# Kernel optimization log

Measured on AMD Instinct MI355X. Metric: run time of the kernel, lower is better.

The kernel has to match this reference:

```python
import jax, jax.numpy as jnp
import numpy as np

R = 15  # receptive-field rows (self.rfield)
_NAMES = ['1x', '2x', '3x', '4x', '1e', '2e', '3e', '4e', '5', '6', '7', '8', '9']
_CIN = [3, 64, 64, 64, 3, 64, 64, 64, 64, 64, 64, 64, 64]
_COUT = [64, 64, 64, 64, 64, 64, 64, 64, 64, 64, 64, 64, 3]


def _leaky(x):
    return jnp.where(x >= 0, x, 0.01 * x)  # nn.LeakyReLU default slope


def _conv(x, w, b, ph):
    # 3x3 conv, stride 1, padding (ph, 1) matching torch Conv2d padding=[ph, 1]
    y = jax.lax.conv_general_dilated(x, w, (1, 1), ((ph, ph), (1, 1)),
                                     dimension_numbers=('NCHW', 'OIHW', 'NCHW'))
    return y + b[None, :, None, None]


def setup_inputs():
    key = jax.random.key(0)
    ks = jax.random.split(key, len(_NAMES) + 1)
    inp = {'x': jax.random.normal(ks[0], (1, 3, 31, 256), jnp.float32)}
    for j, n in enumerate(_NAMES):
        std = np.float32((2.0 / (_CIN[j] * 9)) ** 0.5)  # He init for 3x3 conv
        inp['w' + n] = jax.random.normal(ks[j + 1], (_COUT[j], _CIN[j], 3, 3), jnp.float32) * std
        inp['b' + n] = jnp.zeros((_COUT[j],), jnp.float32)
    return inp


def _predict(s, e, p):
    # x-branch: 15 rows -> 9 rows (three H-valid convs)
    for n, ph in (('1x', 1), ('2x', 0), ('3x', 0), ('4x', 0)):
        s = _leaky(_conv(s, p['w' + n], p['b' + n], ph))
    # e-branch
    for n, ph in (('1e', 1), ('2e', 0), ('3e', 0), ('4e', 0)):
        e = _leaky(_conv(e, p['w' + n], p['b' + n], ph))
    B, C, Hs, W = s.shape  # C == 64 -> per-pixel 8x8 matrices; Hs == R - 6 == 9
    sr = jnp.transpose(s, (0, 2, 3, 1)).reshape(B, Hs, W, 8, 8)
    er = jnp.transpose(e, (0, 2, 3, 1)).reshape(B, Hs, W, 8, 8)
    pr = jnp.einsum('bhwij,bhwjk->bhwik', er, sr).reshape(B, Hs, W, 64)
    pr = jnp.transpose(pr, (0, 3, 1, 2))  # [B,64,9,W]
    # fuse stack: 9 rows -> 1 row, then 64 -> 3 channels
    for n, ph in (('5', 0), ('6', 0), ('7', 0), ('8', 0), ('9', 1)):
        pr = _leaky(_conv(pr, p['w' + n], p['b' + n], ph))
    return pr  # [B, 3, 1, W]


def _forward(x, p):
    B, C, H, W = x.shape

    def step(ebuf, i):
        # torch code sets error = x (alias), so slice_x and slice_e are the SAME mutated buffer
        sl = jax.lax.dynamic_slice(ebuf, (0, 0, i, 0), (B, C, R, W))
        pr = _predict(sl, sl, p)
        # act_row reads row ky of the (mutated) x, but row ky is overwritten only after this read,
        # so it still equals the original input row
        act = jax.lax.dynamic_slice(x, (0, 0, i + R, 0), (B, C, 1, W))
        ebuf = jax.lax.dynamic_update_slice(ebuf, act - pr, (0, 0, i + R, 0))
        return ebuf, pr

    ebuf, preds = jax.lax.scan(step, x, jnp.arange(H - R))
    pred = jnp.transpose(preds[:, :, :, 0, :], (1, 2, 0, 3))  # [S,B,C,1,W] -> [B,C,S,W]
    # 'truth' is read from the in-place-mutated x, i.e. the residual buffer, matching the torch aliasing bug/behavior
    truth = ebuf[:, :, R:, :]
    return pred, truth


def reference(x, w1x, b1x, w2x, b2x, w3x, b3x, w4x, b4x, w1e, b1e, w2e, b2e, w3e, b3e, w4e, b4e, w5, b5, w6, b6, w7, b7, w8, b8, w9, b9):
    p = dict(w1x=w1x, b1x=b1x, w2x=w2x, b2x=b2x, w3x=w3x, b3x=b3x, w4x=w4x, b4x=b4x,
             w1e=w1e, b1e=b1e, w2e=w2e, b2e=b2e, w3e=w3e, b3e=b3e, w4e=w4e, b4e=b4e,
             w5=w5, b5=b5, w6=w6, b6=b6, w7=w7, b7=b7, w8=w8, b8=b8, w9=w9, b9=b9)
    return _forward(x, p)
```

## Files before the change

kernel.cpp:

```cpp
#include <hip/hip_runtime.h>

#define LEAKY(v) ((v) >= 0.f ? (v) : 0.01f * (v))

#define CS   4608
#define ZS1  294912
#define TSL  16
#define BSL  17
#define EBCS 7936

struct JobD { const float* t0; const float* t1; const float* t2; float* o; };
struct IncP { JobD jd[6]; };

__global__ __launch_bounds__(256, 2) void convInc(
    IncP P, const float* __restrict__ W0, const float* __restrict__ B0,
    const float* __restrict__ W1, const float* __restrict__ B1,
    int zsel, int ics, int ocs)
{
    const int lane = threadIdx.x;
    const int y    = threadIdx.y;
    const int q    = blockIdx.x >> 6;
    const int cout = blockIdx.x & 63;
    const int z    = (zsel >> q) & 1;
    const float* W  = (z ? W1 : W0) + cout * 576 + y * 144;
    const float* Bv = z ? B1 : B0;
    const JobD jd  = P.jd[q];
    const int yo   = y * 16 * ics + lane * 4;
    const float* t0 = jd.t0 + yo;
    const float* t1 = jd.t1 + yo;
    const float* t2 = jd.t2 + yo;

    float acc[4] = {};
    #pragma unroll 4
    for (int c = 0; c < 16; ++c) {
        #pragma unroll
        for (int t = 0; t < 3; ++t) {
            const float* rp = (t == 0 ? t0 : (t == 1 ? t1 : t2)) + c * ics;
            float4 v = *(const float4*)rp;
            float wl = __shfl_up(v.w, 1);   if (lane == 0)  wl = 0.f;
            float wr = __shfl_down(v.x, 1); if (lane == 63) wr = 0.f;
            const float win[6] = {wl, v.x, v.y, v.z, v.w, wr};
            const float* wj = W + c * 9 + t * 3;
            #pragma unroll
            for (int cc = 0; cc < 4; ++cc)
                acc[cc] += wj[0] * win[cc] + wj[1] * win[cc + 1] + wj[2] * win[cc + 2];
        }
    }

    __shared__ float red[4][256];
    *(float4*)&red[y][lane * 4] = *(float4*)acc;
    __syncthreads();
    const int col = y * 64 + lane;
    float v = Bv[cout] + red[0][col] + red[1][col] + red[2][col] + red[3][col];
    jd.o[cout * ocs + col] = LEAKY(v);
}

struct C3P { const float* t[3][3]; float* o[3][2]; };

__global__ __launch_bounds__(256, 2) void conv3inc(
    C3P P, const float* __restrict__ W0, const float* __restrict__ B0,
    const float* __restrict__ W1, const float* __restrict__ B1)
{
    const int lane = threadIdx.x & 63;
    const int wv   = threadIdx.x >> 6;
    const int job  = blockIdx.x >> 3;
    const int cq   = blockIdx.x & 3;
    const int z    = (blockIdx.x >> 2) & 1;
    const int cout0 = __builtin_amdgcn_readfirstlane(cq * 16 + wv * 4);
    const float* W  = (z ? W1 : W0) + cout0 * 27;
    const float* Bv = z ? B1 : B0;

    float a[4][4] = {};
    #pragma unroll
    for (int t = 0; t < 3; ++t) {
        const float* rp = P.t[job][t];
        if (rp) {
            #pragma unroll
            for (int c = 0; c < 3; ++c) {
                float4 v = *(const float4*)(rp + c * EBCS + lane * 4);
                float wl = __shfl_up(v.w, 1);   if (lane == 0)  wl = 0.f;
                float wr = __shfl_down(v.x, 1); if (lane == 63) wr = 0.f;
                const float win[6] = {wl, v.x, v.y, v.z, v.w, wr};
                #pragma unroll
                for (int j = 0; j < 4; ++j) {
                    const float* wj = W + j * 27 + c * 9 + t * 3;
                    #pragma unroll
                    for (int cc = 0; cc < 4; ++cc)
                        a[j][cc] += wj[0] * win[cc] + wj[1] * win[cc + 1] + wj[2] * win[cc + 2];
                }
            }
        }
    }
    float* o = P.o[job][z];
    #pragma unroll
    for (int j = 0; j < 4; ++j) {
        const float bb = Bv[cout0 + j];
        float4 r4;
        r4.x = LEAKY(a[j][0] + bb); r4.y = LEAKY(a[j][1] + bb);
        r4.z = LEAKY(a[j][2] + bb); r4.w = LEAKY(a[j][3] + bb);
        *(float4*)(o + (cout0 + j) * CS + lane * 4) = r4;
    }
}

__global__ __launch_bounds__(256, 2) void conv3B(
    const float* __restrict__ ebuf,
    const float* __restrict__ W0, const float* __restrict__ B0,
    const float* __restrict__ W1, const float* __restrict__ B1,
    float* __restrict__ out)
{
    const int lane = threadIdx.x & 63;
    const int wv   = threadIdx.x >> 6;
    const int h  = blockIdx.y;
    const int cq = blockIdx.z & 3;
    const int z  = blockIdx.z >> 2;
    const int cout0 = __builtin_amdgcn_readfirstlane(cq * 16 + wv * 4);
    const float* W  = (z ? W1 : W0) + cout0 * 27;
    const float* Bv = z ? B1 : B0;

    float a[4][4] = {};
    #pragma unroll
    for (int kh = 0; kh < 3; ++kh) {
        const int r = h - 1 + kh;
        const bool valid = (r >= 0 && r < 15);
        const float msk = valid ? 1.f : 0.f;
        #pragma unroll
        for (int c = 0; c < 3; ++c) {
            const float* rr = ebuf + c * EBCS + (valid ? r : 0) * 256 + lane * 4;
            float4 v = *(const float4*)rr;
            v.x *= msk; v.y *= msk; v.z *= msk; v.w *= msk;
            float wl = __shfl_up(v.w, 1);   if (lane == 0)  wl = 0.f;
            float wr = __shfl_down(v.x, 1); if (lane == 63) wr = 0.f;
            const float win[6] = {wl, v.x, v.y, v.z, v.w, wr};
            #pragma unroll
            for (int j = 0; j < 4; ++j) {
                const float* wj = W + j * 27 + c * 9 + kh * 3;
                #pragma unroll
                for (int cc = 0; cc < 4; ++cc)
                    a[j][cc] += wj[0] * win[cc] + wj[1] * win[cc + 1] + wj[2] * win[cc + 2];
            }
        }
    }
    const int slot = (h == 0) ? TSL : (h == 14 ? BSL : (h & 15));
    float* o = out + (size_t)z * ZS1 + slot * 256;
    #pragma unroll
    for (int j = 0; j < 4; ++j) {
        const float bb = Bv[cout0 + j];
        float4 r4;
        r4.x = LEAKY(a[j][0] + bb); r4.y = LEAKY(a[j][1] + bb);
        r4.z = LEAKY(a[j][2] + bb); r4.w = LEAKY(a[j][3] + bb);
        *(float4*)(o + (cout0 + j) * CS + lane * 4) = r4;
    }
}

template<int HOUT, int HIN, int OFFI, int OFFO, int NZ>
__global__ __launch_bounds__(256, 2) void convYB(
    const float* __restrict__ in,
    const float* __restrict__ W0, const float* __restrict__ B0,
    const float* __restrict__ W1, const float* __restrict__ B1,
    float* __restrict__ out)
{
    const int lane = threadIdx.x;
    const int y    = threadIdx.y;
    const int h  = blockIdx.y;
    const int gz = blockIdx.z;
    const int z    = (NZ == 2) ? (gz >> 6) : 0;
    const int cout = (NZ == 2) ? (gz & 63) : gz;
    const float* W  = (z ? W1 : W0) + cout * 576 + y * 144;
    const float* Bv = z ? B1 : B0;
    const float* ib = in + (size_t)z * ZS1 + y * 16 * CS + lane * 4;

    int slot[3];
    #pragma unroll
    for (int t = 0; t < 3; ++t) {
        const int g = h + t;
        slot[t] = (g == 0) ? TSL : (g == HIN - 1 ? BSL : ((g + OFFI) & 15));
    }

    float acc[4] = {};
    #pragma unroll 4
    for (int c = 0; c < 16; ++c) {
        #pragma unroll
        for (int t = 0; t < 3; ++t) {
            float4 v = *(const float4*)(ib + c * CS + slot[t] * 256);
            float wl = __shfl_up(v.w, 1);   if (lane == 0)  wl = 0.f;
            float wr = __shfl_down(v.x, 1); if (lane == 63) wr = 0.f;
            const float win[6] = {wl, v.x, v.y, v.z, v.w, wr};
            const float* wj = W + c * 9 + t * 3;
            #pragma unroll
            for (int cc = 0; cc < 4; ++cc)
                acc[cc] += wj[0] * win[cc] + wj[1] * win[cc + 1] + wj[2] * win[cc + 2];
        }
    }

    __shared__ float red[4][256];
    *(float4*)&red[y][lane * 4] = *(float4*)acc;
    __syncthreads();
    const int col = y * 64 + lane;
    const int os = (h == 0) ? TSL : (h == HOUT - 1 ? BSL : ((h + OFFO) & 15));
    float v = Bv[cout] + red[0][col] + red[1][col] + red[2][col] + red[3][col];
    out[(size_t)z * ZS1 + cout * CS + os * 256 + col] = LEAKY(v);
}

__global__ __launch_bounds__(256, 2) void mmB(const float* __restrict__ L4R,
                                              float* __restrict__ MMR)
{
    const int col = threadIdx.x;
    const int r   = blockIdx.x;
    const int ig  = blockIdx.y;
    const int slot = (r == 0) ? TSL : (r == 8 ? BSL : ((r + 3) & 15));
    const float* s = L4R + slot * 256 + col;
    const float* e = L4R + ZS1 + slot * 256 + col;
    float sv[64];
    #pragma unroll
    for (int c = 0; c < 64; ++c) sv[c] = s[c * CS];
    float ev[8];
    #pragma unroll
    for (int j = 0; j < 8; ++j) ev[j] = e[(ig * 8 + j) * CS];
    #pragma unroll
    for (int k = 0; k < 8; ++k) {
        float acc = 0.f;
        #pragma unroll
        for (int j = 0; j < 8; ++j) acc += ev[j] * sv[j * 8 + k];
        MMR[(ig * 8 + k) * CS + slot * 256 + col] = acc;
    }
}

struct MMP { const float* s[3]; const float* e[3]; float* o[3]; };
__global__ __launch_bounds__(256, 2) void mminc(MMP P)
{
    const int col = threadIdx.x;
    const int job = blockIdx.x;
    const int ig  = blockIdx.y;
    const float* s = P.s[job] + col;
    const float* e = P.e[job] + col;
    float sv[64];
    #pragma unroll
    for (int c = 0; c < 64; ++c) sv[c] = s[c * CS];
    float ev[8];
    #pragma unroll
    for (int j = 0; j < 8; ++j) ev[j] = e[(ig * 8 + j) * CS];
    float* o = P.o[job];
    #pragma unroll
    for (int k = 0; k < 8; ++k) {
        float acc = 0.f;
        #pragma unroll
        for (int j = 0; j < 8; ++j) acc += ev[j] * sv[j * 8 + k];
        o[(ig * 8 + k) * CS + col] = acc;
    }
}

__global__ void conv9up(const float* __restrict__ pin, const float* __restrict__ w9,
                        const float* __restrict__ b9, const float* __restrict__ x,
                        float* __restrict__ ebuf, float* __restrict__ preds, int i)
{
    const int wcol = threadIdx.x;
    const int yq   = threadIdx.y;
    const int c0   = yq * 16;
    const bool mL = (wcol > 0), mR = (wcol < 255);
    float a0 = 0.f, a1 = 0.f, a2 = 0.f;

    #pragma unroll 4
    for (int c = 0; c < 16; ++c) {
        const int cin = c0 + c;
        const float* r_ = pin + cin * 256;
        float vm = mL ? r_[wcol - 1] : 0.f;
        float v0 = r_[wcol];
        float vp = mR ? r_[wcol + 1] : 0.f;
        const float* wk0 = w9 + (0 * 64 + cin) * 9 + 3;
        const float* wk1 = w9 + (1 * 64 + cin) * 9 + 3;
        const float* wk2 = w9 + (2 * 64 + cin) * 9 + 3;
        a0 += vm * wk0[0] + v0 * wk0[1] + vp * wk0[2];
        a1 += vm * wk1[0] + v0 * wk1[1] + vp * wk1[2];
        a2 += vm * wk2[0] + v0 * wk2[1] + vp * wk2[2];
    }

    __shared__ float red[4][3][256];
    red[yq][0][wcol] = a0;
    red[yq][1][wcol] = a1;
    red[yq][2][wcol] = a2;
    __syncthreads();

    if (yq == 0) {
        #pragma unroll
        for (int j = 0; j < 3; ++j) {
            float v = b9[j] + red[0][j][wcol] + red[1][j][wcol]
                            + red[2][j][wcol] + red[3][j][wcol];
            v = LEAKY(v);
            preds[i * 768 + j * 256 + wcol] = v;
            ebuf[j * EBCS + (15 + i) * 256 + wcol] =
                x[j * EBCS + (15 + i) * 256 + wcol] - v;
        }
    }
}

__global__ void finalize(const float* __restrict__ preds, const float* __restrict__ ebuf,
                         float* __restrict__ o)
{
    const int idx = blockIdx.x * 256 + threadIdx.x;
    if (idx >= 24576) return;
    if (idx < 12288) {
        const int c = idx >> 12;
        const int t = (idx >> 8) & 15;
        const int w = idx & 255;
        o[idx] = preds[t * 768 + c * 256 + w];
    } else {
        const int j = idx - 12288;
        const int c = j >> 12;
        const int t = (j >> 8) & 15;
        const int w = j & 255;
        o[idx] = ebuf[c * EBCS + (15 + t) * 256 + w];
    }
}

extern "C" void kernel_launch(void* const* d_in, const int* in_sizes, int n_in,
                              void* d_out, int out_size, void* d_ws, size_t ws_size,
                              hipStream_t stream)
{
    const float* x   = (const float*)d_in[0];
    const float* w1x = (const float*)d_in[1];  const float* b1x = (const float*)d_in[2];
    const float* w2x = (const float*)d_in[3];  const float* b2x = (const float*)d_in[4];
    const float* w3x = (const float*)d_in[5];  const float* b3x = (const float*)d_in[6];
    const float* w4x = (const float*)d_in[7];  const float* b4x = (const float*)d_in[8];
    const float* w1e = (const float*)d_in[9];  const float* b1e = (const float*)d_in[10];
    const float* w2e = (const float*)d_in[11]; const float* b2e = (const float*)d_in[12];
    const float* w3e = (const float*)d_in[13]; const float* b3e = (const float*)d_in[14];
    const float* w4e = (const float*)d_in[15]; const float* b4e = (const float*)d_in[16];
    const float* w5  = (const float*)d_in[17]; const float* b5  = (const float*)d_in[18];
    const float* w6  = (const float*)d_in[19]; const float* b6  = (const float*)d_in[20];
    const float* w7  = (const float*)d_in[21]; const float* b7  = (const float*)d_in[22];
    const float* w8  = (const float*)d_in[23]; const float* b8  = (const float*)d_in[24];
    const float* w9  = (const float*)d_in[25]; const float* b9  = (const float*)d_in[26];

    float* ws    = (float*)d_ws;
    float* ebuf  = ws;
    float* L1R   = ebuf + 23808;
    float* L2R   = L1R + 589824;
    float* L3R   = L2R + 589824;
    float* L4R   = L3R + 589824;
    float* MMR   = L4R + 589824;
    float* L5R   = MMR + 294912;
    float* L6R   = L5R + 294912;
    float* L7b   = L6R + 294912;
    float* L8b   = L7b + 49152;
    float* preds = L8b + 16384;

    auto S2 = [](int c) { return c & 15; };
    auto r2 = [](float* b, int z, int slot) { return b + (size_t)z * ZS1 + slot * 256; };
    auto r1 = [](float* b, int slot) { return b + slot * 256; };

    hipMemcpyAsync(ebuf, x, 23808 * sizeof(float), hipMemcpyDeviceToDevice, stream);

    const dim3 cb(64, 4);

    conv3B<<<dim3(1, 15, 8), 256, 0, stream>>>(ebuf, w1x, b1x, w1e, b1e, L1R);
    convYB<13, 15, 0, 1, 2><<<dim3(1, 13, 128), cb, 0, stream>>>(L1R, w2x, b2x, w2e, b2e, L2R);
    convYB<11, 13, 1, 2, 2><<<dim3(1, 11, 128), cb, 0, stream>>>(L2R, w3x, b3x, w3e, b3e, L3R);
    convYB<9, 11, 2, 3, 2><<<dim3(1, 9, 128), cb, 0, stream>>>(L3R, w4x, b4x, w4e, b4e, L4R);
    mmB<<<dim3(9, 8), 256, 0, stream>>>(L4R, MMR);
    convYB<7, 9, 3, 4, 1><<<dim3(1, 7, 64), cb, 0, stream>>>(MMR, w5, b5, w5, b5, L5R);
    convYB<5, 7, 4, 5, 1><<<dim3(1, 5, 64), cb, 0, stream>>>(L5R, w6, b6, w6, b6, L6R);

    for (int i = 0; i < 16; ++i) {
        if (i > 0) {
            C3P p3 = {};
            p3.t[0][0] = nullptr;                p3.t[0][1] = ebuf + i * 256;        p3.t[0][2] = ebuf + (i + 1) * 256;
            p3.t[1][0] = ebuf + (i + 13) * 256;  p3.t[1][1] = ebuf + (i + 14) * 256; p3.t[1][2] = nullptr;
            p3.t[2][0] = ebuf + (i + 12) * 256;  p3.t[2][1] = ebuf + (i + 13) * 256; p3.t[2][2] = ebuf + (i + 14) * 256;
            for (int z = 0; z < 2; ++z) {
                p3.o[0][z] = r2(L1R, z, TSL);
                p3.o[1][z] = r2(L1R, z, BSL);
                p3.o[2][z] = r2(L1R, z, S2(i + 13));
            }
            conv3inc<<<24, 256, 0, stream>>>(p3, w1x, b1x, w1e, b1e);

            IncP p2 = {};
            for (int z = 0; z < 2; ++z) {
                p2.jd[0 * 2 + z] = { r2(L1R, z, TSL),        r2(L1R, z, S2(i + 1)),  r2(L1R, z, S2(i + 2)),  r2(L2R, z, TSL) };
                p2.jd[1 * 2 + z] = { r2(L1R, z, S2(i + 12)), r2(L1R, z, S2(i + 13)), r2(L1R, z, BSL),        r2(L2R, z, BSL) };
                p2.jd[2 * 2 + z] = { r2(L1R, z, S2(i + 11)), r2(L1R, z, S2(i + 12)), r2(L1R, z, S2(i + 13)), r2(L2R, z, S2(i + 12)) };
            }
            convInc<<<384, cb, 0, stream>>>(p2, w2x, b2x, w2e, b2e, 42, CS, CS);

            IncP p3i = {};
            for (int z = 0; z < 2; ++z) {
                p3i.jd[0 * 2 + z] = { r2(L2R, z, TSL),        r2(L2R, z, S2(i + 2)),  r2(L2R, z, S2(i + 3)),  r2(L3R, z, TSL) };
                p3i.jd[1 * 2 + z] = { r2(L2R, z, S2(i + 11)), r2(L2R, z, S2(i + 12)), r2(L2R, z, BSL),        r2(L3R, z, BSL) };
                p3i.jd[2 * 2 + z] = { r2(L2R, z, S2(i + 10)), r2(L2R, z, S2(i + 11)), r2(L2R, z, S2(i + 12)), r2(L3R, z, S2(i + 11)) };
            }
            convInc<<<384, cb, 0, stream>>>(p3i, w3x, b3x, w3e, b3e, 42, CS, CS);

            IncP p4 = {};
            for (int z = 0; z < 2; ++z) {
                p4.jd[0 * 2 + z] = { r2(L3R, z, TSL),        r2(L3R, z, S2(i + 3)),  r2(L3R, z, S2(i + 4)),  r2(L4R, z, TSL) };
                p4.jd[1 * 2 + z] = { r2(L3R, z, S2(i + 10)), r2(L3R, z, S2(i + 11)), r2(L3R, z, BSL),        r2(L4R, z, BSL) };
                p4.jd[2 * 2 + z] = { r2(L3R, z, S2(i + 9)),  r2(L3R, z, S2(i + 10)), r2(L3R, z, S2(i + 11)), r2(L4R, z, S2(i + 10)) };
            }
            convInc<<<384, cb, 0, stream>>>(p4, w4x, b4x, w4e, b4e, 42, CS, CS);

            MMP pm;
            pm.s[0] = r2(L4R, 0, TSL);        pm.e[0] = r2(L4R, 1, TSL);        pm.o[0] = r1(MMR, TSL);
            pm.s[1] = r2(L4R, 0, BSL);        pm.e[1] = r2(L4R, 1, BSL);        pm.o[1] = r1(MMR, BSL);
            pm.s[2] = r2(L4R, 0, S2(i + 10)); pm.e[2] = r2(L4R, 1, S2(i + 10)); pm.o[2] = r1(MMR, S2(i + 10));
            mminc<<<dim3(3, 8), 256, 0, stream>>>(pm);

            IncP p5 = {};
            p5.jd[0] = { r1(MMR, TSL),       r1(MMR, S2(i + 4)),  r1(MMR, S2(i + 5)),  r1(L5R, TSL) };
            p5.jd[1] = { r1(MMR, S2(i + 9)), r1(MMR, S2(i + 10)), r1(MMR, BSL),        r1(L5R, BSL) };
            p5.jd[2] = { r1(MMR, S2(i + 8)), r1(MMR, S2(i + 9)),  r1(MMR, S2(i + 10)), r1(L5R, S2(i + 9)) };
            convInc<<<192, cb, 0, stream>>>(p5, w5, b5, w5, b5, 0, CS, CS);

            IncP p6 = {};
            p6.jd[0] = { r1(L5R, TSL),       r1(L5R, S2(i + 5)), r1(L5R, S2(i + 6)), r1(L6R, TSL) };
            p6.jd[1] = { r1(L5R, S2(i + 8)), r1(L5R, S2(i + 9)), r1(L5R, BSL),       r1(L6R, BSL) };
            p6.jd[2] = { r1(L5R, S2(i + 7)), r1(L5R, S2(i + 8)), r1(L5R, S2(i + 9)), r1(L6R, S2(i + 8)) };
            convInc<<<192, cb, 0, stream>>>(p6, w6, b6, w6, b6, 0, CS, CS);
        }

        IncP p7 = {};
        p7.jd[0] = { r1(L6R, TSL),       r1(L6R, S2(i + 6)), r1(L6R, S2(i + 7)), L7b };
        p7.jd[1] = { r1(L6R, S2(i + 6)), r1(L6R, S2(i + 7)), r1(L6R, S2(i + 8)), L7b + 256 };
        p7.jd[2] = { r1(L6R, S2(i + 7)), r1(L6R, S2(i + 8)), r1(L6R, BSL),       L7b + 512 };
        convInc<<<192, cb, 0, stream>>>(p7, w7, b7, w7, b7, 0, CS, 768);

        IncP p8 = {};
        p8.jd[0] = { L7b, L7b + 256, L7b + 512, L8b };
        convInc<<<64, cb, 0, stream>>>(p8, w8, b8, w8, b8, 0, 768, 256);

        conv9up<<<dim3(1, 1, 1), dim3(256, 4), 0, stream>>>(L8b, w9, b9, x, ebuf, preds, i);
    }

    finalize<<<96, 256, 0, stream>>>(preds, ebuf, (float*)d_out);
}
```

Baseline: 1.905 ms.

## Replace per-step kernel launches with a persistent kernel using grid barriers

Merges the roughly 144 small per-step launches (conv layers, 8x8 matmul, conv9 update, finalize) into one persistent kernel of 128 workgroups. The workgroups loop over phases and synchronise through a global atomic barrier. This removes launch overhead and inter-kernel gaps on the serial 16-step recurrence. In exchange it needs all workgroups to be co-resident, phases with fewer jobs than workgroups leave most of them idle, and conv9 now runs on a single workgroup at every step.

```diff
diff --git a/kernel.cpp b/kernel.cpp
--- a/kernel.cpp
+++ b/kernel.cpp
@@ -7,99 +7,8 @@
 #define TSL  16
 #define BSL  17
 #define EBCS 7936
-
-struct JobD { const float* t0; const float* t1; const float* t2; float* o; };
-struct IncP { JobD jd[6]; };
-
-__global__ __launch_bounds__(256, 2) void convInc(
-    IncP P, const float* __restrict__ W0, const float* __restrict__ B0,
-    const float* __restrict__ W1, const float* __restrict__ B1,
-    int zsel, int ics, int ocs)
-{
-    const int lane = threadIdx.x;
-    const int y    = threadIdx.y;
-    const int q    = blockIdx.x >> 6;
-    const int cout = blockIdx.x & 63;
-    const int z    = (zsel >> q) & 1;
-    const float* W  = (z ? W1 : W0) + cout * 576 + y * 144;
-    const float* Bv = z ? B1 : B0;
-    const JobD jd  = P.jd[q];
-    const int yo   = y * 16 * ics + lane * 4;
-    const float* t0 = jd.t0 + yo;
-    const float* t1 = jd.t1 + yo;
-    const float* t2 = jd.t2 + yo;
-
-    float acc[4] = {};
-    #pragma unroll 4
-    for (int c = 0; c < 16; ++c) {
-        #pragma unroll
-        for (int t = 0; t < 3; ++t) {
-            const float* rp = (t == 0 ? t0 : (t == 1 ? t1 : t2)) + c * ics;
-            float4 v = *(const float4*)rp;
-            float wl = __shfl_up(v.w, 1);   if (lane == 0)  wl = 0.f;
-            float wr = __shfl_down(v.x, 1); if (lane == 63) wr = 0.f;
-            const float win[6] = {wl, v.x, v.y, v.z, v.w, wr};
-            const float* wj = W + c * 9 + t * 3;
-            #pragma unroll
-            for (int cc = 0; cc < 4; ++cc)
-                acc[cc] += wj[0] * win[cc] + wj[1] * win[cc + 1] + wj[2] * win[cc + 2];
-        }
-    }
-
-    __shared__ float red[4][256];
-    *(float4*)&red[y][lane * 4] = *(float4*)acc;
-    __syncthreads();
-    const int col = y * 64 + lane;
-    float v = Bv[cout] + red[0][col] + red[1][col] + red[2][col] + red[3][col];
-    jd.o[cout * ocs + col] = LEAKY(v);
-}
-
-struct C3P { const float* t[3][3]; float* o[3][2]; };
-
-__global__ __launch_bounds__(256, 2) void conv3inc(
-    C3P P, const float* __restrict__ W0, const float* __restrict__ B0,
-    const float* __restrict__ W1, const float* __restrict__ B1)
-{
-    const int lane = threadIdx.x & 63;
-    const int wv   = threadIdx.x >> 6;
-    const int job  = blockIdx.x >> 3;
-    const int cq   = blockIdx.x & 3;
-    const int z    = (blockIdx.x >> 2) & 1;
-    const int cout0 = __builtin_amdgcn_readfirstlane(cq * 16 + wv * 4);
-    const float* W  = (z ? W1 : W0) + cout0 * 27;
-    const float* Bv = z ? B1 : B0;
-
-    float a[4][4] = {};
-    #pragma unroll
-    for (int t = 0; t < 3; ++t) {
-        const float* rp = P.t[job][t];
-        if (rp) {
-            #pragma unroll
-            for (int c = 0; c < 3; ++c) {
-                float4 v = *(const float4*)(rp + c * EBCS + lane * 4);
-                float wl = __shfl_up(v.w, 1);   if (lane == 0)  wl = 0.f;
-                float wr = __shfl_down(v.x, 1); if (lane == 63) wr = 0.f;
-                const float win[6] = {wl, v.x, v.y, v.z, v.w, wr};
-                #pragma unroll
-                for (int j = 0; j < 4; ++j) {
-                    const float* wj = W + j * 27 + c * 9 + t * 3;
-                    #pragma unroll
-                    for (int cc = 0; cc < 4; ++cc)
-                        a[j][cc] += wj[0] * win[cc] + wj[1] * win[cc + 1] + wj[2] * win[cc + 2];
-                }
-            }
-        }
-    }
-    float* o = P.o[job][z];
-    #pragma unroll
-    for (int j = 0; j < 4; ++j) {
-        const float bb = Bv[cout0 + j];
-        float4 r4;
-        r4.x = LEAKY(a[j][0] + bb); r4.y = LEAKY(a[j][1] + bb);
-        r4.z = LEAKY(a[j][2] + bb); r4.w = LEAKY(a[j][3] + bb);
-        *(float4*)(o + (cout0 + j) * CS + lane * 4) = r4;
-    }
-}
+#define NWG  128
+#define S16(c) ((c) & 15)
 
 __global__ __launch_bounds__(256, 2) void conv3B(
     const float* __restrict__ ebuf,
@@ -112,7 +21,7 @@
     const int h  = blockIdx.y;
     const int cq = blockIdx.z & 3;
     const int z  = blockIdx.z >> 2;
-    const int cout0 = __builtin_amdgcn_readfirstlane(cq * 16 + wv * 4);
+    const int cout0 = cq * 16 + wv * 4;
     const float* W  = (z ? W1 : W0) + cout0 * 27;
     const float* Bv = z ? B1 : B0;
 
@@ -224,90 +133,261 @@
     }
 }
 
-struct MMP { const float* s[3]; const float* e[3]; float* o[3]; };
-__global__ __launch_bounds__(256, 2) void mminc(MMP P)
-{
-    const int col = threadIdx.x;
-    const int job = blockIdx.x;
-    const int ig  = blockIdx.y;
-    const float* s = P.s[job] + col;
-    const float* e = P.e[job] + col;
-    float sv[64];
-    #pragma unroll
-    for (int c = 0; c < 64; ++c) sv[c] = s[c * CS];
-    float ev[8];
-    #pragma unroll
-    for (int j = 0; j < 8; ++j) ev[j] = e[(ig * 8 + j) * CS];
-    float* o = P.o[job];
-    #pragma unroll
-    for (int k = 0; k < 8; ++k) {
-        float acc = 0.f;
-        #pragma unroll
-        for (int j = 0; j < 8; ++j) acc += ev[j] * sv[j * 8 + k];
-        o[(ig * 8 + k) * CS + col] = acc;
-    }
-}
-
-__global__ void conv9up(const float* __restrict__ pin, const float* __restrict__ w9,
-                        const float* __restrict__ b9, const float* __restrict__ x,
-                        float* __restrict__ ebuf, float* __restrict__ preds, int i)
-{
-    const int wcol = threadIdx.x;
-    const int yq   = threadIdx.y;
-    const int c0   = yq * 16;
-    const bool mL = (wcol > 0), mR = (wcol < 255);
-    float a0 = 0.f, a1 = 0.f, a2 = 0.f;
-
+struct SP {
+    const float *x;
+    const float *w1x, *b1x, *w2x, *b2x, *w3x, *b3x, *w4x, *b4x;
+    const float *w1e, *b1e, *w2e, *b2e, *w3e, *b3e, *w4e, *b4e;
+    const float *w5, *b5, *w6, *b6, *w7, *b7, *w8, *b8, *w9, *b9;
+    float *ebuf, *L1R, *L2R, *L3R, *L4R, *MMR, *L5R, *L6R, *L7b, *L8b, *preds, *out;
+    unsigned *bar;
+};
+
+__device__ __forceinline__ void gbar(unsigned* cnt, unsigned* gen)
+{
+    __syncthreads();
+    if (threadIdx.x == 0 && threadIdx.y == 0) {
+        __threadfence();
+        unsigned g = __hip_atomic_load(gen, __ATOMIC_RELAXED, __HIP_MEMORY_SCOPE_AGENT);
+        unsigned v = __hip_atomic_fetch_add(cnt, 1u, __ATOMIC_ACQ_REL, __HIP_MEMORY_SCOPE_AGENT);
+        if (v == NWG - 1) {
+            __hip_atomic_store(cnt, 0u, __ATOMIC_RELAXED, __HIP_MEMORY_SCOPE_AGENT);
+            __hip_atomic_store(gen, g + 1u, __ATOMIC_RELEASE, __HIP_MEMORY_SCOPE_AGENT);
+        } else {
+            while (__hip_atomic_load(gen, __ATOMIC_RELAXED, __HIP_MEMORY_SCOPE_AGENT) == g)
+                __builtin_amdgcn_s_sleep(8);
+        }
+        __threadfence();
+    }
+    __syncthreads();
+}
+
+__device__ __forceinline__ void convRowD(
+    const float* __restrict__ t0, const float* __restrict__ t1, const float* __restrict__ t2,
+    const float* __restrict__ W, float bb, float* __restrict__ orow, int ics,
+    float (*red)[256])
+{
+    const int lane = threadIdx.x, y = threadIdx.y;
+    const float* Wy = W + y * 144;
+    const int yo = y * 16 * ics + lane * 4;
+    const float* p0 = t0 + yo;
+    const float* p1 = t1 + yo;
+    const float* p2 = t2 + yo;
+
+    float acc[4] = {};
     #pragma unroll 4
     for (int c = 0; c < 16; ++c) {
-        const int cin = c0 + c;
-        const float* r_ = pin + cin * 256;
-        float vm = mL ? r_[wcol - 1] : 0.f;
-        float v0 = r_[wcol];
-        float vp = mR ? r_[wcol + 1] : 0.f;
-        const float* wk0 = w9 + (0 * 64 + cin) * 9 + 3;
-        const float* wk1 = w9 + (1 * 64 + cin) * 9 + 3;
-        const float* wk2 = w9 + (2 * 64 + cin) * 9 + 3;
+        #pragma unroll
+        for (int t = 0; t < 3; ++t) {
+            const float* rp = (t == 0 ? p0 : (t == 1 ? p1 : p2)) + c * ics;
+            float4 v = *(const float4*)rp;
+            float wl = __shfl_up(v.w, 1);   if (lane == 0)  wl = 0.f;
+            float wr = __shfl_down(v.x, 1); if (lane == 63) wr = 0.f;
+            const float win[6] = {wl, v.x, v.y, v.z, v.w, wr};
+            const float* wj = Wy + c * 9 + t * 3;
+            #pragma unroll
+            for (int cc = 0; cc < 4; ++cc)
+                acc[cc] += wj[0] * win[cc] + wj[1] * win[cc + 1] + wj[2] * win[cc + 2];
+        }
+    }
+    __syncthreads();
+    *(float4*)&red[y][lane * 4] = *(float4*)acc;
+    __syncthreads();
+    const int col = y * 64 + lane;
+    float v = bb + red[0][col] + red[1][col] + red[2][col] + red[3][col];
+    orow[col] = LEAKY(v);
+}
+
+__device__ __forceinline__ void phaseL1(const SP& p, int i, int wg)
+{
+    const int lane = threadIdx.x, wv = threadIdx.y;
+    for (int vb = wg; vb < 24; vb += NWG) {
+        const int job = vb >> 3, cq = vb & 3, z = (vb >> 2) & 1;
+        const float* taps[3];
+        int os;
+        if (job == 0)      { taps[0] = nullptr;                  taps[1] = p.ebuf + i * 256;        taps[2] = p.ebuf + (i + 1) * 256;  os = TSL; }
+        else if (job == 1) { taps[0] = p.ebuf + (i + 13) * 256;  taps[1] = p.ebuf + (i + 14) * 256; taps[2] = nullptr;                 os = BSL; }
+        else               { taps[0] = p.ebuf + (i + 12) * 256;  taps[1] = p.ebuf + (i + 13) * 256; taps[2] = p.ebuf + (i + 14) * 256; os = S16(i + 13); }
+        const int cout0 = cq * 16 + wv * 4;
+        const float* W  = (z ? p.w1e : p.w1x) + cout0 * 27;
+        const float* Bv = z ? p.b1e : p.b1x;
+
+        float a[4][4] = {};
+        #pragma unroll
+        for (int t = 0; t < 3; ++t) {
+            const float* rp = taps[t];
+            if (rp) {
+                #pragma unroll
+                for (int c = 0; c < 3; ++c) {
+                    float4 v = *(const float4*)(rp + c * EBCS + lane * 4);
+                    float wl = __shfl_up(v.w, 1);   if (lane == 0)  wl = 0.f;
+                    float wr = __shfl_down(v.x, 1); if (lane == 63) wr = 0.f;
+                    const float win[6] = {wl, v.x, v.y, v.z, v.w, wr};
+                    #pragma unroll
+                    for (int j = 0; j < 4; ++j) {
+                        const float* wj = W + j * 27 + c * 9 + t * 3;
+                        #pragma unroll
+                        for (int cc = 0; cc < 4; ++cc)
+                            a[j][cc] += wj[0] * win[cc] + wj[1] * win[cc + 1] + wj[2] * win[cc + 2];
+                    }
+                }
+            }
+        }
+        float* o = p.L1R + (size_t)z * ZS1 + os * 256;
+        #pragma unroll
+        for (int j = 0; j < 4; ++j) {
+            const float bb = Bv[cout0 + j];
+            float4 r4;
+            r4.x = LEAKY(a[j][0] + bb); r4.y = LEAKY(a[j][1] + bb);
+            r4.z = LEAKY(a[j][2] + bb); r4.w = LEAKY(a[j][3] + bb);
+            *(float4*)(o + (cout0 + j) * CS + lane * 4) = r4;
+        }
+    }
+}
+
+__device__ __forceinline__ void phase2t(
+    int i, int d, const float* inR, float* outR,
+    const float* W0, const float* B0, const float* W1, const float* B1,
+    int wg, float (*red)[256])
+{
+    for (int vb = wg; vb < 384; vb += NWG) {
+        const int cout = vb & 63, q = vb >> 6;
+        const int z = q & 1, jt = q >> 1;
+        const float* base = inR + (size_t)z * ZS1;
+        const float* t0; const float* t1; const float* t2; int os;
+        if (jt == 0)      { t0 = base + TSL * 256;              t1 = base + S16(i + d) * 256;      t2 = base + S16(i + d + 1) * 256;  os = TSL; }
+        else if (jt == 1) { t0 = base + S16(i + 13 - d) * 256;  t1 = base + S16(i + 14 - d) * 256; t2 = base + BSL * 256;             os = BSL; }
+        else              { t0 = base + S16(i + 12 - d) * 256;  t1 = base + S16(i + 13 - d) * 256; t2 = base + S16(i + 14 - d) * 256; os = S16(i + 13 - d); }
+        convRowD(t0, t1, t2, (z ? W1 : W0) + cout * 576, (z ? B1 : B0)[cout],
+                 outR + (size_t)z * ZS1 + cout * CS + os * 256, CS, red);
+    }
+}
+
+__device__ __forceinline__ void phase1t(
+    int i, int d, const float* inR, float* outR,
+    const float* W, const float* B, int wg, float (*red)[256])
+{
+    for (int vb = wg; vb < 192; vb += NWG) {
+        const int cout = vb & 63, jt = vb >> 6;
+        const float* t0; const float* t1; const float* t2; int os;
+        if (jt == 0)      { t0 = inR + TSL * 256;              t1 = inR + S16(i + d) * 256;      t2 = inR + S16(i + d + 1) * 256;  os = TSL; }
+        else if (jt == 1) { t0 = inR + S16(i + 13 - d) * 256;  t1 = inR + S16(i + 14 - d) * 256; t2 = inR + BSL * 256;             os = BSL; }
+        else              { t0 = inR + S16(i + 12 - d) * 256;  t1 = inR + S16(i + 13 - d) * 256; t2 = inR + S16(i + 14 - d) * 256; os = S16(i + 13 - d); }
+        convRowD(t0, t1, t2, W + cout * 576, B[cout],
+                 outR + cout * CS + os * 256, CS, red);
+    }
+}
+
+__device__ __forceinline__ void phaseMM(const SP& p, int i, int wg)
+{
+    const int col = threadIdx.y * 64 + threadIdx.x;
+    for (int vb = wg; vb < 24; vb += NWG) {
+        const int job = vb >> 3, ig = vb & 7;
+        const int slot = (job == 0) ? TSL : (job == 1 ? BSL : S16(i + 10));
+        const float* s = p.L4R + slot * 256 + col;
+        const float* e = p.L4R + ZS1 + slot * 256 + col;
+        float sv[64];
+        #pragma unroll
+        for (int c = 0; c < 64; ++c) sv[c] = s[c * CS];
+        float ev[8];
+        #pragma unroll
+        for (int j = 0; j < 8; ++j) ev[j] = e[(ig * 8 + j) * CS];
+        #pragma unroll
+        for (int k = 0; k < 8; ++k) {
+            float acc = 0.f;
+            #pragma unroll
+            for (int j = 0; j < 8; ++j) acc += ev[j] * sv[j * 8 + k];
+            p.MMR[(ig * 8 + k) * CS + slot * 256 + col] = acc;
+        }
+    }
+}
+
+__device__ __forceinline__ void phaseL7(const SP& p, int i, int wg, float (*red)[256])
+{
+    for (int vb = wg; vb < 192; vb += NWG) {
+        const int cout = vb & 63, jt = vb >> 6;
+        const float* t0; const float* t1; const float* t2;
+        if (jt == 0)      { t0 = p.L6R + TSL * 256;          t1 = p.L6R + S16(i + 6) * 256; t2 = p.L6R + S16(i + 7) * 256; }
+        else if (jt == 1) { t0 = p.L6R + S16(i + 6) * 256;   t1 = p.L6R + S16(i + 7) * 256; t2 = p.L6R + S16(i + 8) * 256; }
+        else              { t0 = p.L6R + S16(i + 7) * 256;   t1 = p.L6R + S16(i + 8) * 256; t2 = p.L6R + BSL * 256; }
+        convRowD(t0, t1, t2, p.w7 + cout * 576, p.b7[cout],
+                 p.L7b + jt * 256 + cout * 768, CS, red);
+    }
+}
+
+__device__ __forceinline__ void phaseL8(const SP& p, int wg, float (*red)[256])
+{
+    for (int vb = wg; vb < 64; vb += NWG) {
+        convRowD(p.L7b, p.L7b + 256, p.L7b + 512, p.w8 + vb * 576, p.b8[vb],
+                 p.L8b + vb * 256, 768, red);
+    }
+}
+
+__device__ __forceinline__ void dC9(const SP& p, int i)
+{
+    const int col = threadIdx.y * 64 + threadIdx.x;
+    const bool mL = (col > 0), mR = (col < 255);
+    float a0 = 0.f, a1 = 0.f, a2 = 0.f;
+    #pragma unroll 4
+    for (int cin = 0; cin < 64; ++cin) {
+        const float* r_ = p.L8b + cin * 256;
+        float vm = mL ? r_[col - 1] : 0.f;
+        float v0 = r_[col];
+        float vp = mR ? r_[col + 1] : 0.f;
+        const float* wk0 = p.w9 + (0 * 64 + cin) * 9 + 3;
+        const float* wk1 = p.w9 + (1 * 64 + cin) * 9 + 3;
+        const float* wk2 = p.w9 + (2 * 64 + cin) * 9 + 3;
         a0 += vm * wk0[0] + v0 * wk0[1] + vp * wk0[2];
         a1 += vm * wk1[0] + v0 * wk1[1] + vp * wk1[2];
         a2 += vm * wk2[0] + v0 * wk2[1] + vp * wk2[2];
     }
-
-    __shared__ float red[4][3][256];
-    red[yq][0][wcol] = a0;
-    red[yq][1][wcol] = a1;
-    red[yq][2][wcol] = a2;
-    __syncthreads();
-
-    if (yq == 0) {
-        #pragma unroll
-        for (int j = 0; j < 3; ++j) {
-            float v = b9[j] + red[0][j][wcol] + red[1][j][wcol]
-                            + red[2][j][wcol] + red[3][j][wcol];
-            v = LEAKY(v);
-            preds[i * 768 + j * 256 + wcol] = v;
-            ebuf[j * EBCS + (15 + i) * 256 + wcol] =
-                x[j * EBCS + (15 + i) * 256 + wcol] - v;
-        }
-    }
-}
-
-__global__ void finalize(const float* __restrict__ preds, const float* __restrict__ ebuf,
-                         float* __restrict__ o)
-{
-    const int idx = blockIdx.x * 256 + threadIdx.x;
-    if (idx >= 24576) return;
-    if (idx < 12288) {
-        const int c = idx >> 12;
-        const int t = (idx >> 8) & 15;
-        const int w = idx & 255;
-        o[idx] = preds[t * 768 + c * 256 + w];
-    } else {
-        const int j = idx - 12288;
-        const int c = j >> 12;
-        const int t = (j >> 8) & 15;
-        const int w = j & 255;
-        o[idx] = ebuf[c * EBCS + (15 + t) * 256 + w];
+    const float av[3] = {a0, a1, a2};
+    #pragma unroll
+    for (int j = 0; j < 3; ++j) {
+        float v = LEAKY(p.b9[j] + av[j]);
+        p.preds[i * 768 + j * 256 + col] = v;
+        p.ebuf[j * EBCS + (15 + i) * 256 + col] =
+            p.x[j * EBCS + (15 + i) * 256 + col] - v;
+    }
+}
+
+__global__ __launch_bounds__(256, 2) void stepper(SP p)
+{
+    __shared__ float red[4][256];
+    const int wg = blockIdx.x;
+    const int flat = threadIdx.y * 64 + threadIdx.x;
+    unsigned* cnt = p.bar;
+    unsigned* gen = p.bar + 32;
+
+    phaseL7(p, 0, wg, red);  gbar(cnt, gen);
+    phaseL8(p, wg, red);     gbar(cnt, gen);
+    if (wg == 0) dC9(p, 0);  gbar(cnt, gen);
+
+    for (int i = 1; i < 16; ++i) {
+        phaseL1(p, i, wg);                                                gbar(cnt, gen);
+        phase2t(i, 1, p.L1R, p.L2R, p.w2x, p.b2x, p.w2e, p.b2e, wg, red); gbar(cnt, gen);
+        phase2t(i, 2, p.L2R, p.L3R, p.w3x, p.b3x, p.w3e, p.b3e, wg, red); gbar(cnt, gen);
+        phase2t(i, 3, p.L3R, p.L4R, p.w4x, p.b4x, p.w4e, p.b4e, wg, red); gbar(cnt, gen);
+        phaseMM(p, i, wg);                                                gbar(cnt, gen);
+        phase1t(i, 4, p.MMR, p.L5R, p.w5, p.b5, wg, red);                 gbar(cnt, gen);
+        phase1t(i, 5, p.L5R, p.L6R, p.w6, p.b6, wg, red);                 gbar(cnt, gen);
+        phaseL7(p, i, wg, red);                                           gbar(cnt, gen);
+        phaseL8(p, wg, red);                                              gbar(cnt, gen);
+        if (wg == 0) dC9(p, i);                                           gbar(cnt, gen);
+    }
+
+    for (int idx = wg * 256 + flat; idx < 24576; idx += NWG * 256) {
+        if (idx < 12288) {
+            const int c = idx >> 12;
+            const int t = (idx >> 8) & 15;
+            const int w = idx & 255;
+            p.out[idx] = p.preds[t * 768 + c * 256 + w];
+        } else {
+            const int j = idx - 12288;
+            const int c = j >> 12;
+            const int t = (j >> 8) & 15;
+            const int w = j & 255;
+            p.out[idx] = p.ebuf[c * EBCS + (15 + t) * 256 + w];
+        }
     }
 }
 
@@ -315,118 +395,48 @@
                               void* d_out, int out_size, void* d_ws, size_t ws_size,
                               hipStream_t stream)
 {
-    const float* x   = (const float*)d_in[0];
-    const float* w1x = (const float*)d_in[1];  const float* b1x = (const float*)d_in[2];
-    const float* w2x = (const float*)d_in[3];  const float* b2x = (const float*)d_in[4];
-    const float* w3x = (const float*)d_in[5];  const float* b3x = (const float*)d_in[6];
-    const float* w4x = (const float*)d_in[7];  const float* b4x = (const float*)d_in[8];
-    const float* w1e = (const float*)d_in[9];  const float* b1e = (const float*)d_in[10];
-    const float* w2e = (const float*)d_in[11]; const float* b2e = (const float*)d_in[12];
-    const float* w3e = (const float*)d_in[13]; const float* b3e = (const float*)d_in[14];
-    const float* w4e = (const float*)d_in[15]; const float* b4e = (const float*)d_in[16];
-    const float* w5  = (const float*)d_in[17]; const float* b5  = (const float*)d_in[18];
-    const float* w6  = (const float*)d_in[19]; const float* b6  = (const float*)d_in[20];
-    const float* w7  = (const float*)d_in[21]; const float* b7  = (const float*)d_in[22];
-    const float* w8  = (const float*)d_in[23]; const float* b8  = (const float*)d_in[24];
-    const float* w9  = (const float*)d_in[25]; const float* b9  = (const float*)d_in[26];
-
-    float* ws    = (float*)d_ws;
-    float* ebuf  = ws;
-    float* L1R   = ebuf + 23808;
-    float* L2R   = L1R + 589824;
-    float* L3R   = L2R + 589824;
-    float* L4R   = L3R + 589824;
-    float* MMR   = L4R + 589824;
-    float* L5R   = MMR + 294912;
-    float* L6R   = L5R + 294912;
-    float* L7b   = L6R + 294912;
-    float* L8b   = L7b + 49152;
-    float* preds = L8b + 16384;
-
-    auto S2 = [](int c) { return c & 15; };
-    auto r2 = [](float* b, int z, int slot) { return b + (size_t)z * ZS1 + slot * 256; };
-    auto r1 = [](float* b, int slot) { return b + slot * 256; };
-
-    hipMemcpyAsync(ebuf, x, 23808 * sizeof(float), hipMemcpyDeviceToDevice, stream);
+    SP p;
+    p.x   = (const float*)d_in[0];
+    p.w1x = (const float*)d_in[1];  p.b1x = (const float*)d_in[2];
+    p.w2x = (const float*)d_in[3];  p.b2x = (const float*)d_in[4];
+    p.w3x = (const float*)d_in[5];  p.b3x = (const float*)d_in[6];
+    p.w4x = (const float*)d_in[7];  p.b4x = (const float*)d_in[8];
+    p.w1e = (const float*)d_in[9];  p.b1e = (const float*)d_in[10];
+    p.w2e = (const float*)d_in[11]; p.b2e = (const float*)d_in[12];
+    p.w3e = (const float*)d_in[13]; p.b3e = (const float*)d_in[14];
+    p.w4e = (const float*)d_in[15]; p.b4e = (const float*)d_in[16];
+    p.w5  = (const float*)d_in[17]; p.b5  = (const float*)d_in[18];
+    p.w6  = (const float*)d_in[19]; p.b6  = (const float*)d_in[20];
+    p.w7  = (const float*)d_in[21]; p.b7  = (const float*)d_in[22];
+    p.w8  = (const float*)d_in[23]; p.b8  = (const float*)d_in[24];
+    p.w9  = (const float*)d_in[25]; p.b9  = (const float*)d_in[26];
+
+    float* ws = (float*)d_ws;
+    p.ebuf  = ws;
+    p.L1R   = p.ebuf + 23808;
+    p.L2R   = p.L1R + 589824;
+    p.L3R   = p.L2R + 589824;
+    p.L4R   = p.L3R + 589824;
+    p.MMR   = p.L4R + 589824;
+    p.L5R   = p.MMR + 294912;
+    p.L6R   = p.L5R + 294912;
+    p.L7b   = p.L6R + 294912;
+    p.L8b   = p.L7b + 49152;
+    p.preds = p.L8b + 16384;
+    p.bar   = (unsigned*)(p.preds + 12288);
+    p.out   = (float*)d_out;
+
+    hipMemsetAsync(p.bar, 0, 64 * sizeof(unsigned), stream);
+    hipMemcpyAsync(p.ebuf, p.x, 23808 * sizeof(float), hipMemcpyDeviceToDevice, stream);
 
     const dim3 cb(64, 4);
-
-    conv3B<<<dim3(1, 15, 8), 256, 0, stream>>>(ebuf, w1x, b1x, w1e, b1e, L1R);
-    convYB<13, 15, 0, 1, 2><<<dim3(1, 13, 128), cb, 0, stream>>>(L1R, w2x, b2x, w2e, b2e, L2R);
-    convYB<11, 13, 1, 2, 2><<<dim3(1, 11, 128), cb, 0, stream>>>(L2R, w3x, b3x, w3e, b3e, L3R);
-    convYB<9, 11, 2, 3, 2><<<dim3(1, 9, 128), cb, 0, stream>>>(L3R, w4x, b4x, w4e, b4e, L4R);
-    mmB<<<dim3(9, 8), 256, 0, stream>>>(L4R, MMR);
-    convYB<7, 9, 3, 4, 1><<<dim3(1, 7, 64), cb, 0, stream>>>(MMR, w5, b5, w5, b5, L5R);
-    convYB<5, 7, 4, 5, 1><<<dim3(1, 5, 64), cb, 0, stream>>>(L5R, w6, b6, w6, b6, L6R);
-
-    for (int i = 0; i < 16; ++i) {
-        if (i > 0) {
-            C3P p3 = {};
-            p3.t[0][0] = nullptr;                p3.t[0][1] = ebuf + i * 256;        p3.t[0][2] = ebuf + (i + 1) * 256;
-            p3.t[1][0] = ebuf + (i + 13) * 256;  p3.t[1][1] = ebuf + (i + 14) * 256; p3.t[1][2] = nullptr;
-            p3.t[2][0] = ebuf + (i + 12) * 256;  p3.t[2][1] = ebuf + (i + 13) * 256; p3.t[2][2] = ebuf + (i + 14) * 256;
-            for (int z = 0; z < 2; ++z) {
-                p3.o[0][z] = r2(L1R, z, TSL);
-                p3.o[1][z] = r2(L1R, z, BSL);
-                p3.o[2][z] = r2(L1R, z, S2(i + 13));
-            }
-            conv3inc<<<24, 256, 0, stream>>>(p3, w1x, b1x, w1e, b1e);
-
-            IncP p2 = {};
-            for (int z = 0; z < 2; ++z) {
-                p2.jd[0 * 2 + z] = { r2(L1R, z, TSL),        r2(L1R, z, S2(i + 1)),  r2(L1R, z, S2(i + 2)),  r2(L2R, z, TSL) };
-                p2.jd[1 * 2 + z] = { r2(L1R, z, S2(i + 12)), r2(L1R, z, S2(i + 13)), r2(L1R, z, BSL),        r2(L2R, z, BSL) };
-                p2.jd[2 * 2 + z] = { r2(L1R, z, S2(i + 11)), r2(L1R, z, S2(i + 12)), r2(L1R, z, S2(i + 13)), r2(L2R, z, S2(i + 12)) };
-            }
-            convInc<<<384, cb, 0, stream>>>(p2, w2x, b2x, w2e, b2e, 42, CS, CS);
-
-            IncP p3i = {};
-            for (int z = 0; z < 2; ++z) {
-                p3i.jd[0 * 2 + z] = { r2(L2R, z, TSL),        r2(L2R, z, S2(i + 2)),  r2(L2R, z, S2(i + 3)),  r2(L3R, z, TSL) };
-                p3i.jd[1 * 2 + z] = { r2(L2R, z, S2(i + 11)), r2(L2R, z, S2(i + 12)), r2(L2R, z, BSL),        r2(L3R, z, BSL) };
-                p3i.jd[2 * 2 + z] = { r2(L2R, z, S2(i + 10)), r2(L2R, z, S2(i + 11)), r2(L2R, z, S2(i + 12)), r2(L3R, z, S2(i + 11)) };
-            }
-            convInc<<<384, cb, 0, stream>>>(p3i, w3x, b3x, w3e, b3e, 42, CS, CS);
-
-            IncP p4 = {};
-            for (int z = 0; z < 2; ++z) {
-                p4.jd[0 * 2 + z] = { r2(L3R, z, TSL),        r2(L3R, z, S2(i + 3)),  r2(L3R, z, S2(i + 4)),  r2(L4R, z, TSL) };
-                p4.jd[1 * 2 + z] = { r2(L3R, z, S2(i + 10)), r2(L3R, z, S2(i + 11)), r2(L3R, z, BSL),        r2(L4R, z, BSL) };
-                p4.jd[2 * 2 + z] = { r2(L3R, z, S2(i + 9)),  r2(L3R, z, S2(i + 10)), r2(L3R, z, S2(i + 11)), r2(L4R, z, S2(i + 10)) };
-            }
-            convInc<<<384, cb, 0, stream>>>(p4, w4x, b4x, w4e, b4e, 42, CS, CS);
-
-            MMP pm;
-            pm.s[0] = r2(L4R, 0, TSL);        pm.e[0] = r2(L4R, 1, TSL);        pm.o[0] = r1(MMR, TSL);
-            pm.s[1] = r2(L4R, 0, BSL);        pm.e[1] = r2(L4R, 1, BSL);        pm.o[1] = r1(MMR, BSL);
-            pm.s[2] = r2(L4R, 0, S2(i + 10)); pm.e[2] = r2(L4R, 1, S2(i + 10)); pm.o[2] = r1(MMR, S2(i + 10));
-            mminc<<<dim3(3, 8), 256, 0, stream>>>(pm);
-
-            IncP p5 = {};
-            p5.jd[0] = { r1(MMR, TSL),       r1(MMR, S2(i + 4)),  r1(MMR, S2(i + 5)),  r1(L5R, TSL) };
-            p5.jd[1] = { r1(MMR, S2(i + 9)), r1(MMR, S2(i + 10)), r1(MMR, BSL),        r1(L5R, BSL) };
-            p5.jd[2] = { r1(MMR, S2(i + 8)), r1(MMR, S2(i + 9)),  r1(MMR, S2(i + 10)), r1(L5R, S2(i + 9)) };
-            convInc<<<192, cb, 0, stream>>>(p5, w5, b5, w5, b5, 0, CS, CS);
-
-            IncP p6 = {};
-            p6.jd[0] = { r1(L5R, TSL),       r1(L5R, S2(i + 5)), r1(L5R, S2(i + 6)), r1(L6R, TSL) };
-            p6.jd[1] = { r1(L5R, S2(i + 8)), r1(L5R, S2(i + 9)), r1(L5R, BSL),       r1(L6R, BSL) };
-            p6.jd[2] = { r1(L5R, S2(i + 7)), r1(L5R, S2(i + 8)), r1(L5R, S2(i + 9)), r1(L6R, S2(i + 8)) };
-            convInc<<<192, cb, 0, stream>>>(p6, w6, b6, w6, b6, 0, CS, CS);
-        }
-
-        IncP p7 = {};
-        p7.jd[0] = { r1(L6R, TSL),       r1(L6R, S2(i + 6)), r1(L6R, S2(i + 7)), L7b };
-        p7.jd[1] = { r1(L6R, S2(i + 6)), r1(L6R, S2(i + 7)), r1(L6R, S2(i + 8)), L7b + 256 };
-        p7.jd[2] = { r1(L6R, S2(i + 7)), r1(L6R, S2(i + 8)), r1(L6R, BSL),       L7b + 512 };
-        convInc<<<192, cb, 0, stream>>>(p7, w7, b7, w7, b7, 0, CS, 768);
-
-        IncP p8 = {};
-        p8.jd[0] = { L7b, L7b + 256, L7b + 512, L8b };
-        convInc<<<64, cb, 0, stream>>>(p8, w8, b8, w8, b8, 0, 768, 256);
-
-        conv9up<<<dim3(1, 1, 1), dim3(256, 4), 0, stream>>>(L8b, w9, b9, x, ebuf, preds, i);
-    }
-
-    finalize<<<96, 256, 0, stream>>>(preds, ebuf, (float*)d_out);
-}
+    conv3B<<<dim3(1, 15, 8), 256, 0, stream>>>(p.ebuf, p.w1x, p.b1x, p.w1e, p.b1e, p.L1R);
+    convYB<13, 15, 0, 1, 2><<<dim3(1, 13, 128), cb, 0, stream>>>(p.L1R, p.w2x, p.b2x, p.w2e, p.b2e, p.L2R);
+    convYB<11, 13, 1, 2, 2><<<dim3(1, 11, 128), cb, 0, stream>>>(p.L2R, p.w3x, p.b3x, p.w3e, p.b3e, p.L3R);
+    convYB<9, 11, 2, 3, 2><<<dim3(1, 9, 128), cb, 0, stream>>>(p.L3R, p.w4x, p.b4x, p.w4e, p.b4e, p.L4R);
+    mmB<<<dim3(9, 8), 256, 0, stream>>>(p.L4R, p.MMR);
+    convYB<7, 9, 3, 4, 1><<<dim3(1, 7, 64), cb, 0, stream>>>(p.MMR, p.w5, p.b5, p.w5, p.b5, p.L5R);
+    convYB<5, 7, 4, 5, 1><<<dim3(1, 5, 64), cb, 0, stream>>>(p.L5R, p.w6, p.b6, p.w6, p.b6, p.L6R);
+
+    stepper<<<NWG, cb, 0, stream>>>(p);
+}
```

Measured after the change: 3.887 ms. 2.04x slower.
